# Optimization experiments

Hardware: AMD Instinct MI355X
Metric: run time of the kernel (lower is better)

Reference implementation:

```python
import jax, jax.numpy as jnp
import numpy as np

N, E, HID, H = 50000, 640000, 128, 8
D = HID // H  # out_feat per head


def _dense(x, w, b):
    # torch nn.Linear: y = x @ w.T + b, w shape [out, in]
    return x @ w.T + b


def setup_inputs() -> dict:
    key = jax.random.key(0)
    ks = jax.random.split(key, 24)
    p = lambda k, shape: jax.random.normal(k, shape, dtype=jnp.float32) * 0.05
    inp = {
        "src": jax.random.randint(ks[0], (E,), 0, N, dtype=jnp.int32),
        "dst": jax.random.randint(ks[1], (E,), 0, N, dtype=jnp.int32),
        "bond_embedding": jax.random.normal(ks[2], (E, HID), dtype=jnp.float32),
        "atom_embedding": jax.random.normal(ks[3], (N, HID), dtype=jnp.float32),
        "dist_decay": jax.random.uniform(ks[4], (E, 1), dtype=jnp.float32),
        "k_w": p(ks[5], (HID, HID)), "k_b": p(ks[6], (HID,)),
        "q_w": p(ks[7], (HID, HID)), "q_b": p(ks[8], (HID,)),
        "attn": p(ks[9], (1, H, D)),
        "lin1_w": p(ks[10], (HID, HID)), "lin1_b": p(ks[11], (HID,)),
        "lin2_w": p(ks[12], (HID, HID)), "lin2_b": p(ks[13], (HID,)),
        "r1a_w": p(ks[14], (HID, HID)), "r1a_b": p(ks[15], (HID,)),
        "r1b_w": p(ks[16], (HID, HID)), "r1b_b": p(ks[17], (HID,)),
        "r2a_w": p(ks[18], (HID, HID)), "r2a_b": p(ks[19], (HID,)),
        "r2b_w": p(ks[20], (HID, HID)), "r2b_b": p(ks[21], (HID,)),
    }
    return inp


def reference(src, dst, bond_embedding, atom_embedding, dist_decay,
              k_w, k_b, q_w, q_b, attn,
              lin1_w, lin1_b, lin2_w, lin2_b,
              r1a_w, r1a_b, r1b_w, r1b_b,
              r2a_w, r2a_b, r2b_w, r2b_b):
    n = atom_embedding.shape[0]
    # per-node k/q projections -> [N, H, D]  (feat_drop=0 -> identity)
    k = _dense(atom_embedding, k_w, k_b).reshape(n, H, D)
    q = _dense(atom_embedding, q_w, q_b).reshape(n, H, D)
    # u_add_v gather: e = k[src] + q[dst], then LeakyReLU (slope 0.01)
    e = jax.nn.leaky_relu(k[src] + q[dst], negative_slope=0.01)  # [E,H,D]
    att = jnp.sum(e * attn, axis=-1, keepdims=True)              # [E,H,1]
    z = att + dist_decay[:, None, :]                              # [E,H,1]
    # edge softmax over incoming edges of each destination node (stable)
    zmax = jax.ops.segment_max(z, dst, num_segments=n)            # [N,H,1]
    ez = jnp.exp(z - zmax[dst])
    denom = jax.ops.segment_sum(ez, dst, num_segments=n)          # [N,H,1]
    att_decay = ez / denom[dst]                                   # [E,H,1] (attn_drop=0)
    # weighted scatter-sum of bond messages to nodes
    m = bond_embedding.reshape(-1, H, D) * att_decay              # [E,H,D]
    ft = jax.ops.segment_sum(m, dst, num_segments=n).reshape(n, HID)
    # dense output path + residual with atom_embedding
    he = _dense(jax.nn.relu(_dense(ft, lin1_w, lin1_b)), lin2_w, lin2_b)
    he = he + atom_embedding
    # two residual MLP blocks (ReLU-activated DenseLayers)
    he = he + jax.nn.relu(_dense(jax.nn.relu(_dense(he, r1a_w, r1a_b)), r1b_w, r1b_b))
    he = he + jax.nn.relu(_dense(jax.nn.relu(_dense(he, r2a_w, r2a_b)), r2b_w, r2b_b))
    return he
```

## Files before the change

### kernel.cpp

```cpp
#include <hip/hip_runtime.h>
#include <hip/hip_bf16.h>

#define HID 128
#define NHEAD 8

typedef __attribute__((ext_vector_type(8))) short bf16x8;
typedef __attribute__((ext_vector_type(4))) float f32x4;

__device__ __forceinline__ float bf2f(unsigned short u) {
    return __uint_as_float(((unsigned)u) << 16);
}
__device__ __forceinline__ unsigned short f2bf(float f) {
    unsigned u = __float_as_uint(f);
    unsigned r = ((u >> 16) & 1u) + 0x7FFFu;
    return (unsigned short)((u + r) >> 16);
}

__global__ void cvt_weights_kernel(const float* w0, const float* w1, const float* w2,
                                   const float* w3, const float* w4, const float* w5,
                                   const float* w6, const float* w7,
                                   unsigned short* __restrict__ out) {
    int i = blockIdx.x * 256 + threadIdx.x;
    int m = i >> 14;
    int off = i & 16383;
    const float* w;
    switch (m) {
        case 0: w = w0; break; case 1: w = w1; break;
        case 2: w = w2; break; case 3: w = w3; break;
        case 4: w = w4; break; case 5: w = w5; break;
        case 6: w = w6; break; default: w = w7; break;
    }
    out[i] = f2bf(w[off]);
}

__global__ __launch_bounds__(256) void gemm_kq_kernel(
    const float* __restrict__ A,
    const unsigned short* __restrict__ W,
    const float* __restrict__ b0, const float* __restrict__ b1,
    unsigned short* __restrict__ outb, int R)
{
    const int lane = threadIdx.x & 63;
    const int wv = threadIdx.x >> 6;
    const int row0 = blockIdx.x * 64 + wv * 16;
    if (row0 >= R) return;
    const int rl = lane & 15;
    int arow = row0 + rl; if (arow > R - 1) arow = R - 1;
    const int kchunk = (lane >> 4) * 8;

    f32x4 acc[16];
#pragma unroll
    for (int t = 0; t < 16; ++t) acc[t] = (f32x4){0.f, 0.f, 0.f, 0.f};

#pragma unroll
    for (int kk = 0; kk < 4; ++kk) {
        const int kb = kk * 32 + kchunk;
        float4 x0 = *(const float4*)(A + (size_t)arow * HID + kb);
        float4 x1 = *(const float4*)(A + (size_t)arow * HID + kb + 4);
        bf16x8 a;
        a[0] = (short)f2bf(x0.x); a[1] = (short)f2bf(x0.y);
        a[2] = (short)f2bf(x0.z); a[3] = (short)f2bf(x0.w);
        a[4] = (short)f2bf(x1.x); a[5] = (short)f2bf(x1.y);
        a[6] = (short)f2bf(x1.z); a[7] = (short)f2bf(x1.w);
#pragma unroll
        for (int t = 0; t < 16; ++t) {
            bf16x8 b = *(const bf16x8*)(W + (size_t)(t * 16 + rl) * HID + kb);
            acc[t] = __builtin_amdgcn_mfma_f32_16x16x32_bf16(a, b, acc[t], 0, 0, 0);
        }
    }

    const int rbase = row0 + (lane >> 4) * 4;
#pragma unroll
    for (int i = 0; i < 4; ++i) {
        const int row = rbase + i;
        if (row < R) {
#pragma unroll
            for (int t = 0; t < 16; ++t) {
                const int col = t * 16 + rl;
                float bias = (t < 8) ? b0[col] : b1[col - 128];
                outb[(size_t)row * 256 + col] = f2bf(acc[t][i] + bias);
            }
        }
    }
}

__global__ __launch_bounds__(256) void edge_kernel(
    const int* __restrict__ src, const int* __restrict__ dst,
    const unsigned short* __restrict__ kq, const float* __restrict__ attn,
    const float* __restrict__ dist, float* __restrict__ ez,
    float* __restrict__ denom, int* __restrict__ head, int* __restrict__ nxt, int E)
{
    const int e = blockIdx.x * 16 + (threadIdx.x >> 4);
    if (e >= E) return;
    const int subl = threadIdx.x & 15;
    const int s = src[e], d = dst[e];
    bf16x8 kk8 = *(const bf16x8*)(kq + (size_t)s * 256 + subl * 8);
    bf16x8 qq8 = *(const bf16x8*)(kq + (size_t)d * 256 + 128 + subl * 8);
    float4 at0 = *(const float4*)(attn + subl * 8);
    float4 at1 = *(const float4*)(attn + subl * 8 + 4);
    float p = 0.f;
#pragma unroll
    for (int j = 0; j < 8; ++j) {
        float v = bf2f((unsigned short)kk8[j]) + bf2f((unsigned short)qq8[j]);
        v = v > 0.f ? v : 0.01f * v;
        float aj = (j < 4) ? (&at0.x)[j] : (&at1.x)[j - 4];
        p += v * aj;
    }
    p += __shfl_xor(p, 1);
    if ((subl & 1) == 0) {
        const int h = subl >> 1;
        float ev = __expf(p + dist[e]);
        ez[(size_t)e * NHEAD + h] = ev;
        atomicAdd(&denom[(size_t)d * NHEAD + h], ev);
    }
    if (subl == 0) nxt[e] = atomicExch(&head[d], e);
}

__global__ __launch_bounds__(256) void node_agg_kernel(
    const int* __restrict__ head, const int* __restrict__ nxt,
    const float* __restrict__ ez, const float* __restrict__ denom,
    const float* __restrict__ bond, unsigned short* __restrict__ ft, int N)
{
    const int n = blockIdx.x * 8 + (threadIdx.x >> 5);
    if (n >= N) return;
    const int l = threadIdx.x & 31;
    const int h = l >> 2;
    float a0 = 0.f, a1 = 0.f, a2 = 0.f, a3 = 0.f;
    int e = head[n];
    while (e >= 0) {
        int en = nxt[e];
        float w = ez[(size_t)e * NHEAD + h];
        float4 b = *(const float4*)(bond + (size_t)e * HID + l * 4);
        a0 += w * b.x; a1 += w * b.y; a2 += w * b.z; a3 += w * b.w;
        e = en;
    }
    float dn = denom[(size_t)n * NHEAD + h];
    float di = dn > 0.f ? 1.0f / dn : 0.f;
    ushort4 o;
    o.x = f2bf(a0 * di); o.y = f2bf(a1 * di);
    o.z = f2bf(a2 * di); o.w = f2bf(a3 * di);
    *(ushort4*)(ft + (size_t)n * HID + l * 4) = o;
}

template<bool RELU2, bool WB>
__global__ __launch_bounds__(256) void mlp2_kernel(
    const unsigned short* __restrict__ A,
    const unsigned short* __restrict__ W1, const float* __restrict__ bv1,
    const unsigned short* __restrict__ W2, const float* __restrict__ bv2,
    const float* __restrict__ res,
    float* __restrict__ outf, unsigned short* __restrict__ outb, int R)
{
    __shared__ __align__(16) unsigned short xb[4][16][136];
    const int lane = threadIdx.x & 63;
    const int wv = threadIdx.x >> 6;
    const int row0 = blockIdx.x * 64 + wv * 16;
    const int rl = lane & 15;
    int arow = row0 + rl; if (arow > R - 1) arow = R - 1;
    const int kchunk = (lane >> 4) * 8;
    const int rloc = (lane >> 4) * 4;

    f32x4 acc[8];
#pragma unroll
    for (int t = 0; t < 8; ++t) acc[t] = (f32x4){0.f, 0.f, 0.f, 0.f};
#pragma unroll
    for (int kk = 0; kk < 4; ++kk) {
        const int kb = kk * 32 + kchunk;
        bf16x8 a = *(const bf16x8*)(A + (size_t)arow * HID + kb);
#pragma unroll
        for (int t = 0; t < 8; ++t) {
            bf16x8 b = *(const bf16x8*)(W1 + (size_t)(t * 16 + rl) * HID + kb);
            acc[t] = __builtin_amdgcn_mfma_f32_16x16x32_bf16(a, b, acc[t], 0, 0, 0);
        }
    }
#pragma unroll
    for (int i = 0; i < 4; ++i) {
#pragma unroll
        for (int t = 0; t < 8; ++t) {
            const int col = t * 16 + rl;
            float v = acc[t][i] + bv1[col];
            v = v > 0.f ? v : 0.f;
            xb[wv][rloc + i][col] = f2bf(v);
        }
    }
    __syncthreads();

    f32x4 acc2[8];
#pragma unroll
    for (int t = 0; t < 8; ++t) acc2[t] = (f32x4){0.f, 0.f, 0.f, 0.f};
#pragma unroll
    for (int kk = 0; kk < 4; ++kk) {
        const int kb = kk * 32 + kchunk;
        bf16x8 a2 = *(const bf16x8*)(&xb[wv][rl][kb]);
#pragma unroll
        for (int t = 0; t < 8; ++t) {
            bf16x8 b = *(const bf16x8*)(W2 + (size_t)(t * 16 + rl) * HID + kb);
            acc2[t] = __builtin_amdgcn_mfma_f32_16x16x32_bf16(a2, b, acc2[t], 0, 0, 0);
        }
    }

    const int rbase = row0 + rloc;
#pragma unroll
    for (int i = 0; i < 4; ++i) {
        const int row = rbase + i;
        if (row < R) {
#pragma unroll
            for (int t = 0; t < 8; ++t) {
                const int col = t * 16 + rl;
                float v = acc2[t][i] + bv2[col];
                if (RELU2) v = v > 0.f ? v : 0.f;
                v += res[(size_t)row * HID + col];
                outf[(size_t)row * HID + col] = v;
                if (WB) outb[(size_t)row * HID + col] = f2bf(v);
            }
        }
    }
}

extern "C" void kernel_launch(void* const* d_in, const int* in_sizes, int n_in,
                              void* d_out, int out_size, void* d_ws, size_t ws_size,
                              hipStream_t stream)
{
    const int*   src    = (const int*)d_in[0];
    const int*   dst    = (const int*)d_in[1];
    const float* bond   = (const float*)d_in[2];
    const float* atom   = (const float*)d_in[3];
    const float* dist   = (const float*)d_in[4];
    const float* k_w    = (const float*)d_in[5];
    const float* k_b    = (const float*)d_in[6];
    const float* q_w    = (const float*)d_in[7];
    const float* q_b    = (const float*)d_in[8];
    const float* attn   = (const float*)d_in[9];
    const float* lin1_w = (const float*)d_in[10];
    const float* lin1_b = (const float*)d_in[11];
    const float* lin2_w = (const float*)d_in[12];
    const float* lin2_b = (const float*)d_in[13];
    const float* r1a_w  = (const float*)d_in[14];
    const float* r1a_b  = (const float*)d_in[15];
    const float* r1b_w  = (const float*)d_in[16];
    const float* r1b_b  = (const float*)d_in[17];
    const float* r2a_w  = (const float*)d_in[18];
    const float* r2a_b  = (const float*)d_in[19];
    const float* r2b_w  = (const float*)d_in[20];
    const float* r2b_b  = (const float*)d_in[21];

    const int E = in_sizes[0];
    const int N = in_sizes[3] / HID;

    char* base = (char*)d_ws;
    size_t off = 0;
    auto alloc = [&](size_t bytes) -> char* {
        char* p = base + off;
        off = (off + bytes + 255) & ~(size_t)255;
        return p;
    };
    unsigned short* wbuf = (unsigned short*)alloc((size_t)8 * 16384 * 2);
    unsigned short* kqb  = (unsigned short*)alloc((size_t)N * 256 * 2);
    float*    ezb   = (float*)alloc((size_t)E * NHEAD * 4);
    float*    denom = (float*)alloc((size_t)N * NHEAD * 4);
    int*      head  = (int*)alloc((size_t)N * 4);
    int*      nxt   = (int*)alloc((size_t)E * 4);
    unsigned short* ftb  = (unsigned short*)alloc((size_t)N * HID * 2);
    float*    hef   = (float*)alloc((size_t)N * HID * 4);
    unsigned short* heb  = (unsigned short*)alloc((size_t)N * HID * 2);
    float*    he2f  = (float*)alloc((size_t)N * HID * 4);
    unsigned short* he2b = (unsigned short*)alloc((size_t)N * HID * 2);
    float* out_f = (float*)d_out;

    hipMemsetAsync(denom, 0,    (size_t)N * NHEAD * 4, stream);
    hipMemsetAsync(head,  0xFF, (size_t)N * 4, stream);

    cvt_weights_kernel<<<512, 256, 0, stream>>>(k_w, q_w, lin1_w, lin2_w,
                                                r1a_w, r1b_w, r2a_w, r2b_w, wbuf);

    const int gg = (N + 63) / 64;
    gemm_kq_kernel<<<gg, 256, 0, stream>>>(atom, wbuf, k_b, q_b, kqb, N);

    edge_kernel<<<(E + 15) / 16, 256, 0, stream>>>(src, dst, kqb, attn, dist,
                                                   ezb, denom, head, nxt, E);

    node_agg_kernel<<<(N + 7) / 8, 256, 0, stream>>>(head, nxt, ezb, denom, bond, ftb, N);

    mlp2_kernel<false, true ><<<gg, 256, 0, stream>>>(
        ftb,  wbuf + 2 * 16384, lin1_b, wbuf + 3 * 16384, lin2_b, atom,  hef,  heb,  N);
    mlp2_kernel<true,  true ><<<gg, 256, 0, stream>>>(
        heb,  wbuf + 4 * 16384, r1a_b,  wbuf + 5 * 16384, r1b_b,  hef,   he2f, he2b, N);
    mlp2_kernel<true,  false><<<gg, 256, 0, stream>>>(
        he2b, wbuf + 6 * 16384, r2a_b,  wbuf + 7 * 16384, r2b_b,  he2f,  out_f, nullptr, N);
}
```

Baseline: 739.0 us.

## Fuse three MLP kernels into one and give each edge four lanes

```diff
diff --git a/kernel.cpp b/kernel.cpp
--- a/kernel.cpp
+++ b/kernel.cpp
@@ -89,30 +89,52 @@
     const float* __restrict__ dist, float* __restrict__ ez,
     float* __restrict__ denom, int* __restrict__ head, int* __restrict__ nxt, int E)
 {
-    const int e = blockIdx.x * 16 + (threadIdx.x >> 4);
+    const int e = blockIdx.x * 64 + (threadIdx.x >> 2);
     if (e >= E) return;
-    const int subl = threadIdx.x & 15;
+    const int sub = threadIdx.x & 3;
     const int s = src[e], d = dst[e];
-    bf16x8 kk8 = *(const bf16x8*)(kq + (size_t)s * 256 + subl * 8);
-    bf16x8 qq8 = *(const bf16x8*)(kq + (size_t)d * 256 + 128 + subl * 8);
-    float4 at0 = *(const float4*)(attn + subl * 8);
-    float4 at1 = *(const float4*)(attn + subl * 8 + 4);
-    float p = 0.f;
-#pragma unroll
-    for (int j = 0; j < 8; ++j) {
-        float v = bf2f((unsigned short)kk8[j]) + bf2f((unsigned short)qq8[j]);
-        v = v > 0.f ? v : 0.01f * v;
-        float aj = (j < 4) ? (&at0.x)[j] : (&at1.x)[j - 4];
-        p += v * aj;
-    }
-    p += __shfl_xor(p, 1);
-    if ((subl & 1) == 0) {
-        const int h = subl >> 1;
-        float ev = __expf(p + dist[e]);
-        ez[(size_t)e * NHEAD + h] = ev;
-        atomicAdd(&denom[(size_t)d * NHEAD + h], ev);
-    }
-    if (subl == 0) nxt[e] = atomicExch(&head[d], e);
+    const unsigned short* kp = kq + (size_t)s * 256 + sub * 32;
+    const unsigned short* qp = kq + (size_t)d * 256 + 128 + sub * 32;
+    const float* ap = attn + sub * 32;
+
+    float ph[2];
+#pragma unroll
+    for (int j2 = 0; j2 < 2; ++j2) {
+        bf16x8 kA = *(const bf16x8*)(kp + j2 * 16);
+        bf16x8 kB = *(const bf16x8*)(kp + j2 * 16 + 8);
+        bf16x8 qA = *(const bf16x8*)(qp + j2 * 16);
+        bf16x8 qB = *(const bf16x8*)(qp + j2 * 16 + 8);
+        float av[16];
+#pragma unroll
+        for (int m = 0; m < 4; ++m) {
+            float4 a4 = *(const float4*)(ap + j2 * 16 + m * 4);
+            av[m * 4 + 0] = a4.x; av[m * 4 + 1] = a4.y;
+            av[m * 4 + 2] = a4.z; av[m * 4 + 3] = a4.w;
+        }
+        float p = 0.f;
+#pragma unroll
+        for (int m = 0; m < 8; ++m) {
+            float v = bf2f((unsigned short)kA[m]) + bf2f((unsigned short)qA[m]);
+            v = v > 0.f ? v : 0.01f * v;
+            p += v * av[m];
+        }
+#pragma unroll
+        for (int m = 0; m < 8; ++m) {
+            float v = bf2f((unsigned short)kB[m]) + bf2f((unsigned short)qB[m]);
+            v = v > 0.f ? v : 0.01f * v;
+            p += v * av[8 + m];
+        }
+        ph[j2] = p;
+    }
+    const float dd = dist[e];
+    const float e0 = __expf(ph[0] + dd);
+    const float e1 = __expf(ph[1] + dd);
+    const int h0 = sub * 2;
+    ez[(size_t)e * NHEAD + h0]     = e0;
+    ez[(size_t)e * NHEAD + h0 + 1] = e1;
+    atomicAdd(&denom[(size_t)d * NHEAD + h0],     e0);
+    atomicAdd(&denom[(size_t)d * NHEAD + h0 + 1], e1);
+    if (sub == 0) nxt[e] = atomicExch(&head[d], e);
 }
 
 __global__ __launch_bounds__(256) void node_agg_kernel(
@@ -141,75 +163,127 @@
     *(ushort4*)(ft + (size_t)n * HID + l * 4) = o;
 }
 
-template<bool RELU2, bool WB>
-__global__ __launch_bounds__(256) void mlp2_kernel(
-    const unsigned short* __restrict__ A,
-    const unsigned short* __restrict__ W1, const float* __restrict__ bv1,
-    const unsigned short* __restrict__ W2, const float* __restrict__ bv2,
-    const float* __restrict__ res,
-    float* __restrict__ outf, unsigned short* __restrict__ outb, int R)
-{
-    __shared__ __align__(16) unsigned short xb[4][16][136];
+__device__ __forceinline__ void gemm_pass_lds(const unsigned short* tb,
+                                              const unsigned short* Wm,
+                                              int rl, int g, f32x4 acc[8])
+{
+#pragma unroll
+    for (int t = 0; t < 8; ++t) acc[t] = (f32x4){0.f, 0.f, 0.f, 0.f};
+#pragma unroll
+    for (int kk = 0; kk < 4; ++kk) {
+        const int kb = kk * 32 + g * 8;
+        bf16x8 a = *(const bf16x8*)(tb + rl * 136 + kb);
+#pragma unroll
+        for (int t = 0; t < 8; ++t) {
+            bf16x8 b = *(const bf16x8*)(Wm + (size_t)(t * 16 + rl) * HID + kb);
+            acc[t] = __builtin_amdgcn_mfma_f32_16x16x32_bf16(a, b, acc[t], 0, 0, 0);
+        }
+    }
+}
+
+__device__ __forceinline__ void store_tile_relu(unsigned short* tb, const f32x4 acc[8],
+                                                const float* __restrict__ bias,
+                                                int rl, int g)
+{
+#pragma unroll
+    for (int i = 0; i < 4; ++i) {
+#pragma unroll
+        for (int t = 0; t < 8; ++t) {
+            const int col = t * 16 + rl;
+            float v = acc[t][i] + bias[col];
+            v = v > 0.f ? v : 0.f;
+            tb[(g * 4 + i) * 136 + col] = f2bf(v);
+        }
+    }
+}
+
+__global__ __launch_bounds__(256) void mlp6_kernel(
+    const unsigned short* __restrict__ ftb,
+    const float* __restrict__ atom,
+    const unsigned short* __restrict__ wbuf,
+    const float* __restrict__ b_lin1, const float* __restrict__ b_lin2,
+    const float* __restrict__ b_r1a,  const float* __restrict__ b_r1b,
+    const float* __restrict__ b_r2a,  const float* __restrict__ b_r2b,
+    float* __restrict__ out, int R)
+{
+    __shared__ __align__(16) unsigned short tile[4][16][136];
     const int lane = threadIdx.x & 63;
     const int wv = threadIdx.x >> 6;
     const int row0 = blockIdx.x * 64 + wv * 16;
+    if (row0 >= R) return;
     const int rl = lane & 15;
+    const int g = lane >> 4;
+    unsigned short* tb = &tile[wv][0][0];
     int arow = row0 + rl; if (arow > R - 1) arow = R - 1;
-    const int kchunk = (lane >> 4) * 8;
-    const int rloc = (lane >> 4) * 4;
-
-    f32x4 acc[8];
+
+    const unsigned short* W1 = wbuf + 2 * 16384;
+    const unsigned short* W2 = wbuf + 3 * 16384;
+    const unsigned short* W3 = wbuf + 4 * 16384;
+    const unsigned short* W4 = wbuf + 5 * 16384;
+    const unsigned short* W5 = wbuf + 6 * 16384;
+    const unsigned short* W6 = wbuf + 7 * 16384;
+
+    f32x4 acc[8], carry[8];
+
 #pragma unroll
     for (int t = 0; t < 8; ++t) acc[t] = (f32x4){0.f, 0.f, 0.f, 0.f};
 #pragma unroll
     for (int kk = 0; kk < 4; ++kk) {
-        const int kb = kk * 32 + kchunk;
-        bf16x8 a = *(const bf16x8*)(A + (size_t)arow * HID + kb);
+        const int kb = kk * 32 + g * 8;
+        bf16x8 a = *(const bf16x8*)(ftb + (size_t)arow * HID + kb);
 #pragma unroll
         for (int t = 0; t < 8; ++t) {
             bf16x8 b = *(const bf16x8*)(W1 + (size_t)(t * 16 + rl) * HID + kb);
             acc[t] = __builtin_amdgcn_mfma_f32_16x16x32_bf16(a, b, acc[t], 0, 0, 0);
         }
     }
-#pragma unroll
-    for (int i = 0; i < 4; ++i) {
+    store_tile_relu(tb, acc, b_lin1, rl, g);
+
+    gemm_pass_lds(tb, W2, rl, g, acc);
+#pragma unroll
+    for (int i = 0; i < 4; ++i) {
+        const int row = row0 + g * 4 + i;
+        const int rr = row < R ? row : R - 1;
 #pragma unroll
         for (int t = 0; t < 8; ++t) {
             const int col = t * 16 + rl;
-            float v = acc[t][i] + bv1[col];
+            float v = acc[t][i] + b_lin2[col] + atom[(size_t)rr * HID + col];
+            carry[t][i] = v;
+            tb[(g * 4 + i) * 136 + col] = f2bf(v);
+        }
+    }
+
+    gemm_pass_lds(tb, W3, rl, g, acc);
+    store_tile_relu(tb, acc, b_r1a, rl, g);
+
+    gemm_pass_lds(tb, W4, rl, g, acc);
+#pragma unroll
+    for (int i = 0; i < 4; ++i) {
+#pragma unroll
+        for (int t = 0; t < 8; ++t) {
+            const int col = t * 16 + rl;
+            float v = acc[t][i] + b_r1b[col];
             v = v > 0.f ? v : 0.f;
-            xb[wv][rloc + i][col] = f2bf(v);
-        }
-    }
-    __syncthreads();
-
-    f32x4 acc2[8];
-#pragma unroll
-    for (int t = 0; t < 8; ++t) acc2[t] = (f32x4){0.f, 0.f, 0.f, 0.f};
-#pragma unroll
-    for (int kk = 0; kk < 4; ++kk) {
-        const int kb = kk * 32 + kchunk;
-        bf16x8 a2 = *(const bf16x8*)(&xb[wv][rl][kb]);
-#pragma unroll
-        for (int t = 0; t < 8; ++t) {
-            bf16x8 b = *(const bf16x8*)(W2 + (size_t)(t * 16 + rl) * HID + kb);
-            acc2[t] = __builtin_amdgcn_mfma_f32_16x16x32_bf16(a2, b, acc2[t], 0, 0, 0);
-        }
-    }
-
-    const int rbase = row0 + rloc;
-#pragma unroll
-    for (int i = 0; i < 4; ++i) {
-        const int row = rbase + i;
+            v += carry[t][i];
+            carry[t][i] = v;
+            tb[(g * 4 + i) * 136 + col] = f2bf(v);
+        }
+    }
+
+    gemm_pass_lds(tb, W5, rl, g, acc);
+    store_tile_relu(tb, acc, b_r2a, rl, g);
+
+    gemm_pass_lds(tb, W6, rl, g, acc);
+#pragma unroll
+    for (int i = 0; i < 4; ++i) {
+        const int row = row0 + g * 4 + i;
         if (row < R) {
 #pragma unroll
             for (int t = 0; t < 8; ++t) {
                 const int col = t * 16 + rl;
-                float v = acc2[t][i] + bv2[col];
-                if (RELU2) v = v > 0.f ? v : 0.f;
-                v += res[(size_t)row * HID + col];
-                outf[(size_t)row * HID + col] = v;
-                if (WB) outb[(size_t)row * HID + col] = f2bf(v);
+                float v = acc[t][i] + b_r2b[col];
+                v = v > 0.f ? v : 0.f;
+                out[(size_t)row * HID + col] = v + carry[t][i];
             }
         }
     }
@@ -259,10 +333,6 @@
     int*      head  = (int*)alloc((size_t)N * 4);
     int*      nxt   = (int*)alloc((size_t)E * 4);
     unsigned short* ftb  = (unsigned short*)alloc((size_t)N * HID * 2);
-    float*    hef   = (float*)alloc((size_t)N * HID * 4);
-    unsigned short* heb  = (unsigned short*)alloc((size_t)N * HID * 2);
-    float*    he2f  = (float*)alloc((size_t)N * HID * 4);
-    unsigned short* he2b = (unsigned short*)alloc((size_t)N * HID * 2);
     float* out_f = (float*)d_out;
 
     hipMemsetAsync(denom, 0,    (size_t)N * NHEAD * 4, stream);
@@ -274,15 +344,12 @@
     const int gg = (N + 63) / 64;
     gemm_kq_kernel<<<gg, 256, 0, stream>>>(atom, wbuf, k_b, q_b, kqb, N);
 
-    edge_kernel<<<(E + 15) / 16, 256, 0, stream>>>(src, dst, kqb, attn, dist,
+    edge_kernel<<<(E + 63) / 64, 256, 0, stream>>>(src, dst, kqb, attn, dist,
                                                    ezb, denom, head, nxt, E);
 
     node_agg_kernel<<<(N + 7) / 8, 256, 0, stream>>>(head, nxt, ezb, denom, bond, ftb, N);
 
-    mlp2_kernel<false, true ><<<gg, 256, 0, stream>>>(
-        ftb,  wbuf + 2 * 16384, lin1_b, wbuf + 3 * 16384, lin2_b, atom,  hef,  heb,  N);
-    mlp2_kernel<true,  true ><<<gg, 256, 0, stream>>>(
-        heb,  wbuf + 4 * 16384, r1a_b,  wbuf + 5 * 16384, r1b_b,  hef,   he2f, he2b, N);
-    mlp2_kernel<true,  false><<<gg, 256, 0, stream>>>(
-        he2b, wbuf + 6 * 16384, r2a_b,  wbuf + 7 * 16384, r2b_b,  he2f,  out_f, nullptr, N);
-}
+    mlp6_kernel<<<gg, 256, 0, stream>>>(ftb, atom, wbuf,
+                                        lin1_b, lin2_b, r1a_b, r1b_b, r2a_b, r2b_b,
+                                        out_f, N);
+}
```

Result: no change. 734.0 us (-0.7%).
